# Kernel optimization log

Hardware: AMD Instinct MI355X
Metric: run time of the kernel (lower is better)

Reference implementation:

```python
import jax, jax.numpy as jnp
import numpy as np

N_NODES = 50000


def gcn_conv(x, edge_index, W, b, n_nodes):
    # PyG GCNConv: h = D^{-1/2} (A + I) D^{-1/2} (x @ W) + b
    loops = jnp.arange(n_nodes, dtype=edge_index.dtype)
    src = jnp.concatenate([edge_index[0], loops])
    dst = jnp.concatenate([edge_index[1], loops])
    deg = jax.ops.segment_sum(jnp.ones_like(dst, dtype=x.dtype), dst,
                              num_segments=n_nodes)
    dinv = jnp.where(deg > 0, jax.lax.rsqrt(deg), 0.0)
    norm = dinv[src] * dinv[dst]                      # [E+N]
    h = x @ W                                          # [N, out]
    msg = h[src] * norm[:, None]                       # gather + scale
    out = jax.ops.segment_sum(msg, dst, num_segments=n_nodes)
    return out + b


def setup_inputs() -> dict:
    key = jax.random.key(0)
    ks = jax.random.split(key, 8)
    in_c, hid_c, out_c = 256, 128, 64
    x = jax.random.normal(ks[0], (N_NODES, in_c), dtype=jnp.float32)
    edge_index = jax.random.randint(ks[1], (2, 800000), 0, N_NODES, dtype=jnp.int64)
    pos_edge_index = jax.random.randint(ks[2], (2, 200000), 0, N_NODES, dtype=jnp.int64)
    neg_edge_index = jax.random.randint(ks[3], (2, 200000), 0, N_NES if False else N_NODES, dtype=jnp.int64)
    W1 = jax.random.normal(ks[4], (in_c, hid_c), dtype=jnp.float32) / np.sqrt(in_c)
    b1 = jnp.zeros((hid_c,), dtype=jnp.float32)
    W2 = jax.random.normal(ks[5], (hid_c, out_c), dtype=jnp.float32) / np.sqrt(hid_c)
    b2 = jnp.zeros((out_c,), dtype=jnp.float32)
    return {"x": x, "edge_index": edge_index, "pos_edge_index": pos_edge_index,
            "neg_edge_index": neg_edge_index, "W1": W1, "b1": b1, "W2": W2, "b2": b2}


def reference(x, edge_index, pos_edge_index, neg_edge_index, W1, b1, W2, b2):
    n = x.shape[0]
    h = jax.nn.relu(gcn_conv(x, edge_index, W1, b1, n))
    z = gcn_conv(h, edge_index, W2, b2, n)             # [N, out_c]
    ei = jnp.concatenate([pos_edge_index, neg_edge_index], axis=-1)
    logits = jnp.sum(z[ei[0]] * z[ei[1]], axis=-1)     # [E_pos + E_neg]
    return logits
```

## Files before the change

### kernel.cpp

```cpp
#include <hip/hip_runtime.h>
#include <stdint.h>

constexpr int N_NODES = 50000;
constexpr int E_EDGES = 800000;
constexpr int E_PAIR  = 200000;
constexpr int C_IN    = 256;
constexpr int C_HID   = 128;
constexpr int C_OUT   = 64;
constexpr int SLOT    = 64;

constexpr int NBUCK = 196;
constexpr int BCAP  = 4608;
constexpr int CHUNK = 2048;
constexpr int PREPB = 32;
constexpr int BINAB = (E_EDGES + CHUNK - 1) / CHUNK;
constexpr int GEMM1_BLOCKS = (N_NODES + 63) / 64;

typedef __attribute__((ext_vector_type(8))) _Float16 f16x8;
typedef __attribute__((ext_vector_type(2))) _Float16 f16x2;
typedef __attribute__((ext_vector_type(4))) float f32x4;

__device__ inline uint16_t f2h_bits(float v) {
    union { _Float16 h; uint16_t u; } c; c.h = (_Float16)v;
    return c.u;
}
__device__ inline uint32_t pack2h(float a, float b) {
    return (uint32_t)f2h_bits(a) | ((uint32_t)f2h_bits(b) << 16);
}
__device__ inline void acc_h8(float* a, uint4 v) {
    union { uint4 u; _Float16 h[8]; } c; c.u = v;
#pragma unroll
    for (int i = 0; i < 8; ++i) a[i] += (float)c.h[i];
}
__device__ inline void acc_h8s(float* a, uint4 v, float s) {
    union { uint4 u; _Float16 h[8]; } c; c.u = v;
#pragma unroll
    for (int i = 0; i < 8; ++i) a[i] += (float)c.h[i] * s;
}
__device__ inline float dot_h8(uint4 a, uint4 b) {
    union { uint4 u; f16x2 h[4]; } ca, cb; ca.u = a; cb.u = b;
    float v = 0.f;
#pragma unroll
    for (int i = 0; i < 4; ++i) {
#if __has_builtin(__builtin_amdgcn_fdot2)
        v = __builtin_amdgcn_fdot2(ca.h[i], cb.h[i], v, false);
#else
        v += (float)ca.h[i][0] * (float)cb.h[i][0]
           + (float)ca.h[i][1] * (float)cb.h[i][1];
#endif
    }
    return v;
}

template<int N>
__device__ inline int wswz_idx(int k, int n) {
    int c = k >> 5, kq = (k >> 3) & 3, kk = k & 7, ct = n >> 4, nn = n & 15;
    return (((c * (N / 16) + ct) * 4 + kq) * 16 + nn) * 8 + kk;
}

__global__ __launch_bounds__(256) void prep_binA_kernel(
        const float* __restrict__ W1, const float* __restrict__ W2,
        uint16_t* __restrict__ s1, uint16_t* __restrict__ s2,
        const int* __restrict__ src, const int* __restrict__ dst,
        int* __restrict__ gcur, uint32_t* __restrict__ ebuf) {
    __shared__ int cnt[NBUCK], loc[NBUCK], lim[NBUCK], abase[NBUCK], wcur[NBUCK];
    __shared__ int tot;
    __shared__ uint32_t stag[CHUNK];
    __shared__ uint8_t  bof[CHUNK];

    const int t = threadIdx.x;

    if (blockIdx.x < PREPB) {
        for (int id = blockIdx.x * 256 + t;
             id < C_IN * C_HID + C_HID * C_OUT; id += PREPB * 256) {
            if (id < C_IN * C_HID) {
                int idx = wswz_idx<C_HID>(id / C_HID, id & (C_HID - 1));
                s1[idx] = f2h_bits(W1[id]);
            } else {
                int id2 = id - C_IN * C_HID;
                int idx = wswz_idx<C_OUT>(id2 / C_OUT, id2 & (C_OUT - 1));
                s2[idx] = f2h_bits(W2[id2]);
            }
        }
        return;
    }

    const int e0 = (blockIdx.x - PREPB) * CHUNK;
    const int n  = min(CHUNK, E_EDGES - e0);

    for (int b = t; b < NBUCK; b += 256) cnt[b] = 0;
    if (t == 0) tot = 0;
    __syncthreads();

    uint32_t pk[CHUNK / 256]; int bk[CHUNK / 256];
    int ne = 0;
    for (int j = t; j < n; j += 256) {
        int d = dst[e0 + j], s = src[e0 + j];
        int b = d >> 8;
        pk[ne] = ((uint32_t)(d & 255) << 16) | (uint32_t)s;
        bk[ne] = b;
        atomicAdd(&cnt[b], 1);
        ++ne;
    }
    __syncthreads();
    for (int b = t; b < NBUCK; b += 256)
        loc[b] = atomicAdd(&tot, cnt[b]);
    __syncthreads();
    for (int b = t; b < NBUCK; b += 256) {
        int base = atomicAdd(&gcur[b], cnt[b]);
        int room = BCAP - base; if (room < 0) room = 0;
        lim[b]   = loc[b] + room;
        abase[b] = b * BCAP + base - loc[b];
        wcur[b]  = loc[b];
    }
    __syncthreads();
#pragma unroll
    for (int i = 0; i < CHUNK / 256; ++i) {
        if (i < ne) {
            int p = atomicAdd(&wcur[bk[i]], 1);
            stag[p] = pk[i];
            bof[p]  = (uint8_t)bk[i];
        }
    }
    __syncthreads();
    for (int j = t; j < n; j += 256) {
        int b = bof[j];
        if (j < lim[b]) ebuf[abase[b] + j] = stag[j];
    }
}

__global__ __launch_bounds__(256, 3) void build_gemm_kernel(
        const int* __restrict__ gcur, const uint32_t* __restrict__ ebuf,
        uint16_t* __restrict__ col2, int* __restrict__ degc,
        float* __restrict__ dinv,
        const float* __restrict__ A, const uint16_t* __restrict__ Bswz,
        uint16_t* __restrict__ out) {
    constexpr int K = C_IN, N = C_HID;
    constexpr int BM = 64, BK = 32;
    constexpr int CT   = N / 32;
    constexpr int NSUB = N / 16;
    constexpr int ABYTES = BM * BK * 2;
    constexpr int BBYTES = NSUB * 1024;
    __shared__ char sm[ABYTES + BBYTES];

    const int t = threadIdx.x;

    if (blockIdx.x < NBUCK) {
        int* cur = (int*)sm;
        const int b = blockIdx.x;
        cur[t] = 0;
        __syncthreads();

        int cn = gcur[b]; if (cn > BCAP) cn = BCAP;
        const uint32_t* eb = ebuf + (size_t)b * BCAP;
        const size_t nbase = (size_t)b << 8;

        int j = t;
        for (; j + 3 * 256 < cn; j += 4 * 256) {
            uint32_t v0 = eb[j], v1 = eb[j + 256], v2 = eb[j + 512], v3 = eb[j + 768];
            int p0 = atomicAdd(&cur[v0 >> 16], 1);
            int p1 = atomicAdd(&cur[v1 >> 16], 1);
            int p2 = atomicAdd(&cur[v2 >> 16], 1);
            int p3 = atomicAdd(&cur[v3 >> 16], 1);
            if (p0 < SLOT) col2[((nbase + (v0 >> 16)) << 6) + p0] = (uint16_t)(v0 & 0xffff);
            if (p1 < SLOT) col2[((nbase + (v1 >> 16)) << 6) + p1] = (uint16_t)(v1 & 0xffff);
            if (p2 < SLOT) col2[((nbase + (v2 >> 16)) << 6) + p2] = (uint16_t)(v2 & 0xffff);
            if (p3 < SLOT) col2[((nbase + (v3 >> 16)) << 6) + p3] = (uint16_t)(v3 & 0xffff);
        }
        for (; j < cn; j += 256) {
            uint32_t v = eb[j];
            int p = atomicAdd(&cur[v >> 16], 1);
            if (p < SLOT) col2[((nbase + (v >> 16)) << 6) + p] = (uint16_t)(v & 0xffff);
        }
        __syncthreads();
        int node = (int)nbase + t;
        if (node < N_NODES) {
            int dg = cur[t];
            degc[node] = dg;
            dinv[node] = rsqrtf((float)dg + 1.0f);
        }
        return;
    }

    char* As = sm;
    char* Bs = sm + ABYTES;

    const int lane = t & 63;
    const int w    = t >> 6;
    const int wrow = w & 1, wcol = w >> 1;
    const int m0   = (blockIdx.x - NBUCK) * BM;
    const int M    = N_NODES;

    const int sr = t >> 2, skq = t & 3;
    int arow = m0 + sr; if (arow > M - 1) arow = M - 1;
    const float* aptr = A + (size_t)arow * K + skq * 8;
    const int aslot = ((sr >> 4) * 64 + skq * 16 + (sr & 15)) * 16;

    f32x4 acc[2][CT];
#pragma unroll
    for (int rt = 0; rt < 2; ++rt)
#pragma unroll
        for (int ct = 0; ct < CT; ++ct) {
            f32x4 z = {0.f, 0.f, 0.f, 0.f};
            acc[rt][ct] = z;
        }

    const uint4* gh = (const uint4*)Bswz;

    constexpr int NCH = K / BK;
#pragma unroll 1
    for (int c = 0; c < NCH; ++c) {
        float4 v0 = *(const float4*)(aptr + c * BK);
        float4 v1 = *(const float4*)(aptr + c * BK + 4);
        uint4 bh0, bh1;
        {
            const uint4* ch = gh + (size_t)c * (BBYTES / 16);
            bh0 = ch[t];
            bh1 = ch[t + 256];
        }
        __syncthreads();
        {
            float e[8] = {v0.x, v0.y, v0.z, v0.w, v1.x, v1.y, v1.z, v1.w};
            uint32_t hp[4];
#pragma unroll
            for (int j = 0; j < 4; ++j)
                hp[j] = pack2h(e[2 * j], e[2 * j + 1]);
            *(uint4*)(As + aslot) = make_uint4(hp[0], hp[1], hp[2], hp[3]);
        }
        *(uint4*)(Bs + t * 16) = bh0;
        *(uint4*)(Bs + (t + 256) * 16) = bh1;
        __syncthreads();
        f16x8 Ah[2];
#pragma unroll
        for (int rt = 0; rt < 2; ++rt) {
            int st = wrow * 2 + rt;
            Ah[rt] = *(const f16x8*)(As + st * 1024 + lane * 16);
        }
#pragma unroll
        for (int ct = 0; ct < CT; ++ct) {
            int cg = wcol * CT + ct;
            f16x8 Bh = *(const f16x8*)(Bs + cg * 1024 + lane * 16);
#pragma unroll
            for (int rt = 0; rt < 2; ++rt)
                acc[rt][ct] = __builtin_amdgcn_mfma_f32_16x16x32_f16(Ah[rt], Bh, acc[rt][ct], 0, 0, 0);
        }
    }

#pragma unroll
    for (int rt = 0; rt < 2; ++rt) {
        int rowbase = m0 + wrow * 32 + rt * 16 + (lane >> 4) * 4;
#pragma unroll
        for (int ct = 0; ct < CT; ++ct) {
            int n = (wcol * CT + ct) * 16 + (lane & 15);
#pragma unroll
            for (int r = 0; r < 4; ++r) {
                int m = rowbase + r;
                if (m < M) out[(size_t)m * N + n] = f2h_bits(acc[rt][ct][r]);
            }
        }
    }
}

__global__ __launch_bounds__(256) void gather_gemm_kernel(
        const uint16_t* __restrict__ col2, const int* __restrict__ degc,
        const uint16_t* __restrict__ h0u, const float* __restrict__ dinv,
        const float* __restrict__ bias, const uint16_t* __restrict__ B2swz,
        uint16_t* __restrict__ z0s) {
    __shared__ uint4 hlds[256];
    const int t    = threadIdx.x;
    const int lane = t & 63;
    const int w    = t >> 6;
    const int sub  = lane >> 4;
    const int l    = lane & 15;
    const int node_loc = w * 4 + sub;
    const int node = blockIdx.x * 16 + node_loc;

    int dg = degc[node]; if (dg > SLOT) dg = SLOT;
    const float dn = dinv[node];
    const uint4* hs4 = (const uint4*)h0u;
    float a0[8], a1[8];
#pragma unroll
    for (int i = 0; i < 8; ++i) { a0[i] = 0.f; a1[i] = 0.f; }
    {
        uint4 self = hs4[(size_t)node * 16 + l];
        acc_h8s(a0, self, dn);
    }
    const uint32_t* cp = (const uint32_t*)col2;
    const int pbase = node * (SLOT / 2);
    const int sb    = sub * 16;

    for (int c = 0; c * 16 < dg; ++c) {
        int cnt = dg - c * 16; if (cnt > 16) cnt = 16;
        uint32_t cv = (2 * l < cnt) ? cp[pbase + c * 8 + l] : 0u;
        int j = 0;
        for (; j + 8 <= cnt; j += 8) {
            uint32_t p0 = (uint32_t)__shfl((int)cv, sb + (j >> 1),     64);
            uint32_t p1 = (uint32_t)__shfl((int)cv, sb + (j >> 1) + 1, 64);
            uint32_t p2 = (uint32_t)__shfl((int)cv, sb + (j >> 1) + 2, 64);
            uint32_t p3 = (uint32_t)__shfl((int)cv, sb + (j >> 1) + 3, 64);
            int s0 = p0 & 0xffff, s1 = p0 >> 16;
            int s2 = p1 & 0xffff, s3 = p1 >> 16;
            int s4 = p2 & 0xffff, s5 = p2 >> 16;
            int s6 = p3 & 0xffff, s7 = p3 >> 16;
            uint4 v0 = hs4[(size_t)s0 * 16 + l];
            uint4 v1 = hs4[(size_t)s1 * 16 + l];
            uint4 v2 = hs4[(size_t)s2 * 16 + l];
            uint4 v3 = hs4[(size_t)s3 * 16 + l];
            uint4 v4 = hs4[(size_t)s4 * 16 + l];
            uint4 v5 = hs4[(size_t)s5 * 16 + l];
            uint4 v6 = hs4[(size_t)s6 * 16 + l];
            uint4 v7 = hs4[(size_t)s7 * 16 + l];
            float d0 = dinv[s0], d1 = dinv[s1], d2 = dinv[s2], d3 = dinv[s3];
            float d4 = dinv[s4], d5 = dinv[s5], d6 = dinv[s6], d7 = dinv[s7];
            acc_h8s(a0, v0, d0); acc_h8s(a1, v1, d1);
            acc_h8s(a0, v2, d2); acc_h8s(a1, v3, d3);
            acc_h8s(a0, v4, d4); acc_h8s(a1, v5, d5);
            acc_h8s(a0, v6, d6); acc_h8s(a1, v7, d7);
        }
        for (; j + 4 <= cnt; j += 4) {
            uint32_t p0 = (uint32_t)__shfl((int)cv, sb + (j >> 1),     64);
            uint32_t p1 = (uint32_t)__shfl((int)cv, sb + (j >> 1) + 1, 64);
            int s0 = p0 & 0xffff, s1 = p0 >> 16;
            int s2 = p1 & 0xffff, s3 = p1 >> 16;
            uint4 v0 = hs4[(size_t)s0 * 16 + l];
            uint4 v1 = hs4[(size_t)s1 * 16 + l];
            uint4 v2 = hs4[(size_t)s2 * 16 + l];
            uint4 v3 = hs4[(size_t)s3 * 16 + l];
            float d0 = dinv[s0], d1 = dinv[s1], d2 = dinv[s2], d3 = dinv[s3];
            acc_h8s(a0, v0, d0); acc_h8s(a1, v1, d1);
            acc_h8s(a0, v2, d2); acc_h8s(a1, v3, d3);
        }
        for (; j < cnt; ++j) {
            uint32_t p = (uint32_t)__shfl((int)cv, sb + (j >> 1), 64);
            int s = (j & 1) ? (int)(p >> 16) : (int)(p & 0xffff);
            uint4 v = hs4[(size_t)s * 16 + l];
            acc_h8s(a0, v, dinv[s]);
        }
    }
    {
        float4 bb0 = ((const float4*)bias)[2 * l];
        float4 bb1 = ((const float4*)bias)[2 * l + 1];
        float o[8];
        o[0] = fmaxf((a0[0] + a1[0]) * dn + bb0.x, 0.f);
        o[1] = fmaxf((a0[1] + a1[1]) * dn + bb0.y, 0.f);
        o[2] = fmaxf((a0[2] + a1[2]) * dn + bb0.z, 0.f);
        o[3] = fmaxf((a0[3] + a1[3]) * dn + bb0.w, 0.f);
        o[4] = fmaxf((a0[4] + a1[4]) * dn + bb1.x, 0.f);
        o[5] = fmaxf((a0[5] + a1[5]) * dn + bb1.y, 0.f);
        o[6] = fmaxf((a0[6] + a1[6]) * dn + bb1.z, 0.f);
        o[7] = fmaxf((a0[7] + a1[7]) * dn + bb1.w, 0.f);
        hlds[l * 16 + node_loc] = make_uint4(
            pack2h(o[0], o[1]), pack2h(o[2], o[3]),
            pack2h(o[4], o[5]), pack2h(o[6], o[7]));
    }
    __syncthreads();

    f32x4 acc = {0.f, 0.f, 0.f, 0.f};
    const char* hb = (const char*)hlds;
#pragma unroll
    for (int c = 0; c < 4; ++c) {
        f16x8 Af = *(const f16x8*)(hb + c * 1024 + lane * 16);
        f16x8 Bh = *(const f16x8*)(B2swz + (c * 4 + w) * 512 + lane * 8);
        acc = __builtin_amdgcn_mfma_f32_16x16x32_f16(Af, Bh, acc, 0, 0, 0);
    }
    const int colg = w * 16 + (lane & 15);
    const int rowb = blockIdx.x * 16 + (lane >> 4) * 4;
#pragma unroll
    for (int r = 0; r < 4; ++r) {
        int m = rowb + r;
        z0s[(size_t)m * C_OUT + colg] = f2h_bits(acc[r] * dinv[m]);
    }
}

template<int F, bool RELU>
__global__ __launch_bounds__(256) void gather_kernel(
        const uint16_t* __restrict__ col2, const int* __restrict__ degc,
        const uint16_t* __restrict__ hs, const float* __restrict__ dinv,
        const float* __restrict__ bias, uint16_t* __restrict__ out) {
    constexpr int LPN = F / 8;
    constexpr int NPW = 64 / LPN;
    const int lane = threadIdx.x & 63;
    const int sub  = lane / LPN;
    const int l    = lane % LPN;
    const int node = blockIdx.x * (4 * NPW) + (threadIdx.x >> 6) * NPW + sub;
    if (node >= N_NODES) return;

    int dg = degc[node]; if (dg > SLOT) dg = SLOT;
    const uint4* hs4 = (const uint4*)hs;

    float a0[8], a1[8];
#pragma unroll
    for (int i = 0; i < 8; ++i) { a0[i] = 0.f; a1[i] = 0.f; }
    {
        uint4 self = hs4[(size_t)node * LPN + l];
        acc_h8(a0, self);
    }
    const uint32_t* cp = (const uint32_t*)col2;
    const int pbase = node * (SLOT / 2);
    const int sb    = sub * LPN;

    for (int c = 0; c * LPN < dg; ++c) {
        int cnt = dg - c * LPN; if (cnt > LPN) cnt = LPN;
        uint32_t cv = (2 * l < cnt) ? cp[pbase + c * (LPN / 2) + l] : 0u;
        int j = 0;
        for (; j + 8 <= cnt; j += 8) {
            uint32_t p0 = (uint32_t)__shfl((int)cv, sb + (j >> 1),     64);
            uint32_t p1 = (uint32_t)__shfl((int)cv, sb + (j >> 1) + 1, 64);
            uint32_t p2 = (uint32_t)__shfl((int)cv, sb + (j >> 1) + 2, 64);
            uint32_t p3 = (uint32_t)__shfl((int)cv, sb + (j >> 1) + 3, 64);
            int s0 = p0 & 0xffff, s1 = p0 >> 16;
            int s2 = p1 & 0xffff, s3 = p1 >> 16;
            int s4 = p2 & 0xffff, s5 = p2 >> 16;
            int s6 = p3 & 0xffff, s7 = p3 >> 16;
            uint4 v0 = hs4[(size_t)s0 * LPN + l];
            uint4 v1 = hs4[(size_t)s1 * LPN + l];
            uint4 v2 = hs4[(size_t)s2 * LPN + l];
            uint4 v3 = hs4[(size_t)s3 * LPN + l];
            uint4 v4 = hs4[(size_t)s4 * LPN + l];
            uint4 v5 = hs4[(size_t)s5 * LPN + l];
            uint4 v6 = hs4[(size_t)s6 * LPN + l];
            uint4 v7 = hs4[(size_t)s7 * LPN + l];
            acc_h8(a0, v0); acc_h8(a1, v1);
            acc_h8(a0, v2); acc_h8(a1, v3);
            acc_h8(a0, v4); acc_h8(a1, v5);
            acc_h8(a0, v6); acc_h8(a1, v7);
        }
        for (; j + 4 <= cnt; j += 4) {
            uint32_t p0 = (uint32_t)__shfl((int)cv, sb + (j >> 1),     64);
            uint32_t p1 = (uint32_t)__shfl((int)cv, sb + (j >> 1) + 1, 64);
            int s0 = p0 & 0xffff, s1 = p0 >> 16;
            int s2 = p1 & 0xffff, s3 = p1 >> 16;
            uint4 v0 = hs4[(size_t)s0 * LPN + l];
            uint4 v1 = hs4[(size_t)s1 * LPN + l];
            uint4 v2 = hs4[(size_t)s2 * LPN + l];
            uint4 v3 = hs4[(size_t)s3 * LPN + l];
            acc_h8(a0, v0); acc_h8(a1, v1);
            acc_h8(a0, v2); acc_h8(a1, v3);
        }
        for (; j < cnt; ++j) {
            uint32_t p = (uint32_t)__shfl((int)cv, sb + (j >> 1), 64);
            int s = (j & 1) ? (int)(p >> 16) : (int)(p & 0xffff);
            uint4 v = hs4[(size_t)s * LPN + l];
            acc_h8(a0, v);
        }
    }

    const float dn = dinv[node];
    float4 bb0 = ((const float4*)bias)[2 * l];
    float4 bb1 = ((const float4*)bias)[2 * l + 1];
    float o[8];
    o[0] = (a0[0] + a1[0]) * dn + bb0.x;
    o[1] = (a0[1] + a1[1]) * dn + bb0.y;
    o[2] = (a0[2] + a1[2]) * dn + bb0.z;
    o[3] = (a0[3] + a1[3]) * dn + bb0.w;
    o[4] = (a0[4] + a1[4]) * dn + bb1.x;
    o[5] = (a0[5] + a1[5]) * dn + bb1.y;
    o[6] = (a0[6] + a1[6]) * dn + bb1.z;
    o[7] = (a0[7] + a1[7]) * dn + bb1.w;
    if (RELU) {
#pragma unroll
        for (int i = 0; i < 8; ++i) o[i] = fmaxf(o[i], 0.f);
    }
    uint4 res = make_uint4(pack2h(o[0], o[1]), pack2h(o[2], o[3]),
                           pack2h(o[4], o[5]), pack2h(o[6], o[7]));
    ((uint4*)out)[(size_t)node * LPN + l] = res;
}

__global__ __launch_bounds__(256) void logits_kernel(
        const int* __restrict__ pos, const int* __restrict__ neg,
        const uint16_t* __restrict__ z, float* __restrict__ out) {
    const int t = threadIdx.x;
    const int l = t & 7;
    const int g = (blockIdx.x * 256 + t) >> 3;
    const int e0 = 2 * g;
    if (e0 >= 2 * E_PAIR) return;
    int s0, d0, s1, d1;
    if (e0 < E_PAIR) { s0 = pos[e0];          d0 = pos[E_PAIR + e0]; }
    else             { s0 = neg[e0 - E_PAIR]; d0 = neg[e0];          }
    int e1 = e0 + 1;
    if (e1 < E_PAIR) { s1 = pos[e1];          d1 = pos[E_PAIR + e1]; }
    else             { s1 = neg[e1 - E_PAIR]; d1 = neg[e1];          }
    const uint4* z4 = (const uint4*)z;
    uint4 ua0 = z4[(size_t)s0 * 8 + l];
    uint4 ub0 = z4[(size_t)d0 * 8 + l];
    uint4 ua1 = z4[(size_t)s1 * 8 + l];
    uint4 ub1 = z4[(size_t)d1 * 8 + l];
    float v0 = dot_h8(ua0, ub0);
    float v1 = dot_h8(ua1, ub1);
    v0 += __shfl_xor(v0, 1, 64); v1 += __shfl_xor(v1, 1, 64);
    v0 += __shfl_xor(v0, 2, 64); v1 += __shfl_xor(v1, 2, 64);
    v0 += __shfl_xor(v0, 4, 64); v1 += __shfl_xor(v1, 4, 64);
    if (l == 0) { out[e0] = v0; out[e1] = v1; }
}

extern "C" void kernel_launch(void* const* d_in, const int* in_sizes, int n_in,
                              void* d_out, int out_size, void* d_ws, size_t ws_size,
                              hipStream_t stream) {
    const float* x   = (const float*)d_in[0];
    const int*   ei  = (const int*)d_in[1];
    const int*   pos = (const int*)d_in[2];
    const int*   neg = (const int*)d_in[3];
    const float* W1  = (const float*)d_in[4];
    const float* b1  = (const float*)d_in[5];
    const float* W2  = (const float*)d_in[6];
    const float* b2  = (const float*)d_in[7];
    float* out = (float*)d_out;

    const int* src = ei;
    const int* dst = ei + E_EDGES;

    char* ws = (char*)d_ws;
    int*      degc  = (int*)ws;
    float*    dinv  = (float*)(ws + 200704);
    uint16_t* col2  = (uint16_t*)(ws + 401408);
    int*      gcur  = (int*)(ws + 6801408);
    uint16_t* B1swz = (uint16_t*)(ws + 6802432);
    uint16_t* B2swz = (uint16_t*)(ws + 6933504);
    uint16_t* h0u   = (uint16_t*)(ws + 6966272);
    uint16_t* z0s   = (uint16_t*)(ws + 32566272);
    uint16_t* zbuf  = (uint16_t*)(ws + 38966272);
    uint32_t* ebuf  = (uint32_t*)(ws + 45366272);

    hipMemsetAsync(gcur, 0, NBUCK * sizeof(int), stream);

    prep_binA_kernel<<<PREPB + BINAB, 256, 0, stream>>>(
        W1, W2, B1swz, B2swz, src, dst, gcur, ebuf);

    build_gemm_kernel<<<NBUCK + GEMM1_BLOCKS, 256, 0, stream>>>(
        gcur, ebuf, col2, degc, dinv, x, B1swz, h0u);

    gather_gemm_kernel<<<N_NODES / 16, 256, 0, stream>>>(
        col2, degc, h0u, dinv, b1, B2swz, z0s);

    gather_kernel<C_OUT, false><<<(N_NODES + 31) / 32, 256, 0, stream>>>(
        col2, degc, z0s, dinv, b2, zbuf);

    logits_kernel<<<(E_PAIR * 8 + 255) / 256, 256, 0, stream>>>(pos, neg, zbuf, out);
}
```

Before: 198.0 us.

## Stage CSR columns in LDS, pack bucket id into edge word, larger bin chunk

```diff
diff --git a/kernel.cpp b/kernel.cpp
--- a/kernel.cpp
+++ b/kernel.cpp
@@ -11,7 +11,7 @@
 
 constexpr int NBUCK = 196;
 constexpr int BCAP  = 4608;
-constexpr int CHUNK = 2048;
+constexpr int CHUNK = 4096;
 constexpr int PREPB = 32;
 constexpr int BINAB = (E_EDGES + CHUNK - 1) / CHUNK;
 constexpr int GEMM1_BLOCKS = (N_NODES + 63) / 64;
@@ -66,7 +66,6 @@
     __shared__ int cnt[NBUCK], loc[NBUCK], lim[NBUCK], abase[NBUCK], wcur[NBUCK];
     __shared__ int tot;
     __shared__ uint32_t stag[CHUNK];
-    __shared__ uint8_t  bof[CHUNK];
 
     const int t = threadIdx.x;
 
@@ -92,13 +91,12 @@
     if (t == 0) tot = 0;
     __syncthreads();
 
-    uint32_t pk[CHUNK / 256]; int bk[CHUNK / 256];
+    uint32_t pk[CHUNK / 256];
     int ne = 0;
     for (int j = t; j < n; j += 256) {
         int d = dst[e0 + j], s = src[e0 + j];
         int b = d >> 8;
-        pk[ne] = ((uint32_t)(d & 255) << 16) | (uint32_t)s;
-        bk[ne] = b;
+        pk[ne] = ((uint32_t)b << 24) | ((uint32_t)(d & 255) << 16) | (uint32_t)s;
         atomicAdd(&cnt[b], 1);
         ++ne;
     }
@@ -117,15 +115,15 @@
 #pragma unroll
     for (int i = 0; i < CHUNK / 256; ++i) {
         if (i < ne) {
-            int p = atomicAdd(&wcur[bk[i]], 1);
+            int p = atomicAdd(&wcur[pk[i] >> 24], 1);
             stag[p] = pk[i];
-            bof[p]  = (uint8_t)bk[i];
         }
     }
     __syncthreads();
     for (int j = t; j < n; j += 256) {
-        int b = bof[j];
-        if (j < lim[b]) ebuf[abase[b] + j] = stag[j];
+        uint32_t v = stag[j];
+        int b = v >> 24;
+        if (j < lim[b]) ebuf[abase[b] + j] = v & 0x00ffffffu;
     }
 }
 
@@ -141,19 +139,20 @@
     constexpr int NSUB = N / 16;
     constexpr int ABYTES = BM * BK * 2;
     constexpr int BBYTES = NSUB * 1024;
-    __shared__ char sm[ABYTES + BBYTES];
+    __shared__ char sm[1024 + 256 * SLOT * 2];
 
     const int t = threadIdx.x;
 
     if (blockIdx.x < NBUCK) {
         int* cur = (int*)sm;
+        uint16_t* colL = (uint16_t*)(sm + 1024);
         const int b = blockIdx.x;
         cur[t] = 0;
         __syncthreads();
 
         int cn = gcur[b]; if (cn > BCAP) cn = BCAP;
         const uint32_t* eb = ebuf + (size_t)b * BCAP;
-        const size_t nbase = (size_t)b << 8;
+        const int nbase = b << 8;
 
         int j = t;
         for (; j + 3 * 256 < cn; j += 4 * 256) {
@@ -162,18 +161,23 @@
             int p1 = atomicAdd(&cur[v1 >> 16], 1);
             int p2 = atomicAdd(&cur[v2 >> 16], 1);
             int p3 = atomicAdd(&cur[v3 >> 16], 1);
-            if (p0 < SLOT) col2[((nbase + (v0 >> 16)) << 6) + p0] = (uint16_t)(v0 & 0xffff);
-            if (p1 < SLOT) col2[((nbase + (v1 >> 16)) << 6) + p1] = (uint16_t)(v1 & 0xffff);
-            if (p2 < SLOT) col2[((nbase + (v2 >> 16)) << 6) + p2] = (uint16_t)(v2 & 0xffff);
-            if (p3 < SLOT) col2[((nbase + (v3 >> 16)) << 6) + p3] = (uint16_t)(v3 & 0xffff);
+            if (p0 < SLOT) colL[((v0 >> 16) << 6) + p0] = (uint16_t)(v0 & 0xffff);
+            if (p1 < SLOT) colL[((v1 >> 16) << 6) + p1] = (uint16_t)(v1 & 0xffff);
+            if (p2 < SLOT) colL[((v2 >> 16) << 6) + p2] = (uint16_t)(v2 & 0xffff);
+            if (p3 < SLOT) colL[((v3 >> 16) << 6) + p3] = (uint16_t)(v3 & 0xffff);
         }
         for (; j < cn; j += 256) {
             uint32_t v = eb[j];
             int p = atomicAdd(&cur[v >> 16], 1);
-            if (p < SLOT) col2[((nbase + (v >> 16)) << 6) + p] = (uint16_t)(v & 0xffff);
+            if (p < SLOT) colL[((v >> 16) << 6) + p] = (uint16_t)(v & 0xffff);
         }
         __syncthreads();
-        int node = (int)nbase + t;
+        int nodes = N_NODES - nbase; if (nodes > 256) nodes = 256;
+        uint4* dstc = (uint4*)(col2 + ((size_t)nbase << 6));
+        const uint4* srcc = (const uint4*)colL;
+        for (int i = t; i < nodes * 8; i += 256)
+            dstc[i] = srcc[i];
+        int node = nbase + t;
         if (node < N_NODES) {
             int dg = cur[t];
             degc[node] = dg;
```

After: 190.5 us (median of 2 runs). 3.8% less time.
